# Kernel optimization log

Measured on AMD Instinct MI355X. Metric: run time of the kernel, lower is better.

Reference implementation:

```python
import jax, jax.numpy as jnp
import numpy as np

V, D, M, C, L = 100000, 256, 4096, 4096, 32
PAD = 0
EPS = 1e-8  # torch CosineSimilarity default eps


def setup_inputs() -> dict:
    key = jax.random.key(0)
    ks = jax.random.split(key, 6)
    xs = jax.random.randint(ks[0], (1, L), 0, V)
    mems = jax.random.randint(ks[1], (M, L), 0, V)
    ys = jax.random.randint(ks[2], (1, L), 0, V)
    cands = jax.random.randint(ks[3], (C, L), 0, V)
    lt = jax.random.normal(ks[4], (V, D), dtype=jnp.float32) * 0.02
    lt = lt.at[PAD].set(0.0)  # nn.Embedding padding_idx row is zero
    freqs = jax.random.uniform(ks[5], (V,), dtype=jnp.float32, minval=0.05, maxval=1.0)
    return {"xs": xs, "mems": mems, "ys": ys, "cands": cands, "lt": lt, "freqs": freqs}


def _encode(tokens, lt, freqs):
    # Batched Encoder.forward: freq-weighted average of token embeddings.
    # tokens: [N, L] -> [N, D]
    emb = lt[tokens]                       # [N, L, D] gather
    w = freqs[tokens]                      # [N, L]
    w = w / jnp.linalg.norm(w, axis=1, keepdims=True)  # w * (1 / ||w||)
    return jnp.einsum('nl,nld->nd', w, emb)


def reference(xs, mems, ys, cands, lt, freqs):
    xs_emb = _encode(xs, lt, freqs)                                   # [1, D]
    mems_enc = jnp.concatenate([_encode(mems, lt, freqs), xs_emb], 0)  # [M+1, D]
    # cosine similarity of xs_emb (broadcast) against each memory row
    an = jnp.maximum(jnp.linalg.norm(xs_emb, axis=1), EPS)            # [1]
    bn = jnp.maximum(jnp.linalg.norm(mems_enc, axis=1), EPS)          # [M+1]
    cos = (mems_enc @ xs_emb[0]) / (an * bn)                          # [M+1]
    att = jax.nn.softmax(cos)[None, :]                                # [1, M+1]
    lhs_emb = att @ mems_enc                                          # [1, D]
    ys_emb = _encode(ys, lt, freqs)                                   # [1, D]
    cand_emb = _encode(cands, lt, freqs)                              # [C, D]
    # torch.cat of lhs_emb repeated (1 + C) times; ys then cand encodings
    xs_out = jnp.tile(lhs_emb, (cands.shape[0] + 1, 1))               # [C+1, D]
    ys_out = jnp.concatenate([ys_emb, cand_emb], axis=0)              # [C+1, D]
    return xs_out, ys_out
```

## Files before the change

kernel.cpp:

```cpp
#include <hip/hip_runtime.h>

#define V_ 100000
#define D_ 256
#define M_ 4096
#define C_ 4096
#define L_ 32
#define ROWS_MEMS (M_ + 1)
#define NTASK (1 + M_ + 1 + C_)

__device__ __forceinline__ float wave_allreduce_sum(float v) {
    #pragma unroll
    for (int off = 32; off >= 1; off >>= 1) v += __shfl_xor(v, off, 64);
    return v;
}

__global__ __launch_bounds__(256) void encode_fused(
    const int* __restrict__ xs, const int* __restrict__ mems,
    const int* __restrict__ ys, const int* __restrict__ cands,
    const float* __restrict__ lt, const float* __restrict__ freqs,
    float* __restrict__ lhs_raw,
    float* __restrict__ gsum,
    float* __restrict__ out_ys)
{
    __shared__ float s_xf[D_];
    __shared__ float s_an2;
    __shared__ float s_lred[D_];
    __shared__ float s_ered;

    const int wave = threadIdx.x >> 6;
    const int lane = threadIdx.x & 63;
    const int d0 = lane * 4;
    const int rt0 = blockIdx.x * 4;
    const bool block_has_att = (rt0 <= M_);

    s_lred[threadIdx.x] = 0.f;
    if (threadIdx.x == 0) s_ered = 0.f;

    if (block_has_att && wave == 0) {
        int txs = 0; float wxs = 0.f;
        if (lane < L_) { txs = xs[lane]; wxs = freqs[txs]; }
        const float sx = wave_allreduce_sum(wxs * wxs);
        const float wnx = wxs / sqrtf(sx);
        float4 xf = make_float4(0.f, 0.f, 0.f, 0.f);
        #pragma unroll
        for (int l = 0; l < L_; ++l) {
            const int t = __shfl(txs, l, 64);
            const float wl = __shfl(wnx, l, 64);
            const float4 v = *reinterpret_cast<const float4*>(lt + (size_t)t * D_ + d0);
            xf.x += wl * v.x; xf.y += wl * v.y; xf.z += wl * v.z; xf.w += wl * v.w;
        }
        *reinterpret_cast<float4*>(&s_xf[d0]) = xf;
        const float an2 = wave_allreduce_sum(xf.x*xf.x + xf.y*xf.y + xf.z*xf.z + xf.w*xf.w);
        if (lane == 0) s_an2 = an2;
    }
    __syncthreads();

    const int rt = rt0 + wave;
    if (rt < NTASK) {
        const int* tok_ptr; float* dst = nullptr; bool has_att = false;
        if (rt == 0) {
            tok_ptr = xs; has_att = true;
        } else if (rt <= M_) {
            tok_ptr = mems + (size_t)(rt - 1) * L_; has_att = true;
        } else if (rt == M_ + 1) {
            tok_ptr = ys; dst = out_ys;
        } else {
            const int c = rt - (M_ + 2);
            tok_ptr = cands + (size_t)c * L_;
            dst = out_ys + (size_t)(c + 1) * D_;
        }

        int tok = 0; float w = 0.f;
        if (lane < L_) { tok = tok_ptr[lane]; w = freqs[tok]; }
        const float s2 = wave_allreduce_sum(w * w);
        const float wn = w / sqrtf(s2);

        float4 acc = make_float4(0.f, 0.f, 0.f, 0.f);
        #pragma unroll
        for (int l = 0; l < L_; ++l) {
            const int t = __shfl(tok, l, 64);
            const float wl = __shfl(wn, l, 64);
            const float4 v = *reinterpret_cast<const float4*>(lt + (size_t)t * D_ + d0);
            acc.x += wl * v.x; acc.y += wl * v.y; acc.z += wl * v.z; acc.w += wl * v.w;
        }

        if (has_att) {
            const float4 xf = *reinterpret_cast<const float4*>(&s_xf[d0]);
            const float d = wave_allreduce_sum(acc.x*xf.x + acc.y*xf.y + acc.z*xf.z + acc.w*xf.w);
            const float q = wave_allreduce_sum(acc.x*acc.x + acc.y*acc.y + acc.z*acc.z + acc.w*acc.w);
            const float an = fmaxf(sqrtf(s_an2), 1e-8f);
            const float bn = fmaxf(sqrtf(q),  1e-8f);
            const float e = expf(d / (an * bn));
            atomicAdd(&s_lred[d0 + 0], e * acc.x);
            atomicAdd(&s_lred[d0 + 1], e * acc.y);
            atomicAdd(&s_lred[d0 + 2], e * acc.z);
            atomicAdd(&s_lred[d0 + 3], e * acc.w);
            if (lane == 0) atomicAdd(&s_ered, e);
        } else {
            *reinterpret_cast<float4*>(dst + d0) = acc;
        }
    }

    if (block_has_att) {
        __syncthreads();
        atomicAdd(&lhs_raw[threadIdx.x], s_lred[threadIdx.x]);
        if (threadIdx.x == 0) atomicAdd(gsum, s_ered);
    }
}

__global__ __launch_bounds__(256) void finalize_tile(
    const float* __restrict__ lhs_raw, const float* __restrict__ gsum,
    float* __restrict__ out_xs)
{
    const float val = lhs_raw[threadIdx.x] / gsum[0];
    for (int r = blockIdx.x; r < ROWS_MEMS; r += gridDim.x)
        out_xs[(size_t)r * D_ + threadIdx.x] = val;
}

extern "C" void kernel_launch(void* const* d_in, const int* in_sizes, int n_in,
                              void* d_out, int out_size, void* d_ws, size_t ws_size,
                              hipStream_t stream) {
    const int*   xs    = (const int*)d_in[0];
    const int*   mems  = (const int*)d_in[1];
    const int*   ys    = (const int*)d_in[2];
    const int*   cands = (const int*)d_in[3];
    const float* lt    = (const float*)d_in[4];
    const float* freqs = (const float*)d_in[5];

    float* out    = (float*)d_out;
    float* out_xs = out;
    float* out_ys = out + (size_t)ROWS_MEMS * D_;

    float* lhs_raw = (float*)d_ws;
    float* gsum    = lhs_raw + D_;

    hipMemsetAsync(lhs_raw, 0, (D_ + 1) * sizeof(float), stream);

    encode_fused<<<(NTASK + 3) / 4, 256, 0, stream>>>(xs, mems, ys, cands, lt, freqs,
                                                      lhs_raw, gsum, out_ys);
    finalize_tile<<<1024, 256, 0, stream>>>(lhs_raw, gsum, out_xs);
}
```

Baseline: 188.5 us.

## Process two encode tasks per wave and compute norms with scalar loads

The fused encode kernel now launches half as many blocks, and each wave handles two rows: one from the first half of the task range and one candidate row from the second half. Their gather loops are interleaved to expose more independent memory loads per wave. Token weights are now read with uniform per-row scalar loads in place of lane loads plus shuffles. Every block recomputes the xs encoding and always does the shared-memory and global atomic reduction, which adds redundant work and atomics in blocks that have no attention rows. Fewer waves in flight may reduce latency hiding.

```diff
diff --git a/kernel.cpp b/kernel.cpp
--- a/kernel.cpp
+++ b/kernel.cpp
@@ -7,6 +7,8 @@
 #define L_ 32
 #define ROWS_MEMS (M_ + 1)
 #define NTASK (1 + M_ + 1 + C_)
+#define NBLK 1025
+#define HALF (NBLK * 4)
 
 __device__ __forceinline__ float wave_allreduce_sum(float v) {
     #pragma unroll
@@ -14,7 +16,7 @@
     return v;
 }
 
-__global__ __launch_bounds__(256) void encode_fused(
+__global__ __launch_bounds__(256, 4) void encode_fused(
     const int* __restrict__ xs, const int* __restrict__ mems,
     const int* __restrict__ ys, const int* __restrict__ cands,
     const float* __restrict__ lt, const float* __restrict__ freqs,
@@ -30,22 +32,21 @@
     const int wave = threadIdx.x >> 6;
     const int lane = threadIdx.x & 63;
     const int d0 = lane * 4;
-    const int rt0 = blockIdx.x * 4;
-    const bool block_has_att = (rt0 <= M_);
+    const int g = blockIdx.x * 4 + wave;
 
     s_lred[threadIdx.x] = 0.f;
     if (threadIdx.x == 0) s_ered = 0.f;
 
-    if (block_has_att && wave == 0) {
-        int txs = 0; float wxs = 0.f;
-        if (lane < L_) { txs = xs[lane]; wxs = freqs[txs]; }
-        const float sx = wave_allreduce_sum(wxs * wxs);
-        const float wnx = wxs / sqrtf(sx);
+    if (wave == 0) {
+        float s2 = 0.f;
+        #pragma unroll
+        for (int l = 0; l < L_; ++l) { const float w = freqs[xs[l]]; s2 += w * w; }
+        const float inv = 1.0f / sqrtf(s2);
         float4 xf = make_float4(0.f, 0.f, 0.f, 0.f);
         #pragma unroll
         for (int l = 0; l < L_; ++l) {
-            const int t = __shfl(txs, l, 64);
-            const float wl = __shfl(wnx, l, 64);
+            const int t = xs[l];
+            const float wl = freqs[t] * inv;
             const float4 v = *reinterpret_cast<const float4*>(lt + (size_t)t * D_ + d0);
             xf.x += wl * v.x; xf.y += wl * v.y; xf.z += wl * v.z; xf.w += wl * v.w;
         }
@@ -55,57 +56,69 @@
     }
     __syncthreads();
 
-    const int rt = rt0 + wave;
-    if (rt < NTASK) {
-        const int* tok_ptr; float* dst = nullptr; bool has_att = false;
-        if (rt == 0) {
-            tok_ptr = xs; has_att = true;
-        } else if (rt <= M_) {
-            tok_ptr = mems + (size_t)(rt - 1) * L_; has_att = true;
-        } else if (rt == M_ + 1) {
-            tok_ptr = ys; dst = out_ys;
-        } else {
-            const int c = rt - (M_ + 2);
-            tok_ptr = cands + (size_t)c * L_;
-            dst = out_ys + (size_t)(c + 1) * D_;
-        }
-
-        int tok = 0; float w = 0.f;
-        if (lane < L_) { tok = tok_ptr[lane]; w = freqs[tok]; }
-        const float s2 = wave_allreduce_sum(w * w);
-        const float wn = w / sqrtf(s2);
-
-        float4 acc = make_float4(0.f, 0.f, 0.f, 0.f);
-        #pragma unroll
-        for (int l = 0; l < L_; ++l) {
-            const int t = __shfl(tok, l, 64);
-            const float wl = __shfl(wn, l, 64);
-            const float4 v = *reinterpret_cast<const float4*>(lt + (size_t)t * D_ + d0);
-            acc.x += wl * v.x; acc.y += wl * v.y; acc.z += wl * v.z; acc.w += wl * v.w;
-        }
-
-        if (has_att) {
-            const float4 xf = *reinterpret_cast<const float4*>(&s_xf[d0]);
-            const float d = wave_allreduce_sum(acc.x*xf.x + acc.y*xf.y + acc.z*xf.z + acc.w*xf.w);
-            const float q = wave_allreduce_sum(acc.x*acc.x + acc.y*acc.y + acc.z*acc.z + acc.w*acc.w);
-            const float an = fmaxf(sqrtf(s_an2), 1e-8f);
-            const float bn = fmaxf(sqrtf(q),  1e-8f);
-            const float e = expf(d / (an * bn));
-            atomicAdd(&s_lred[d0 + 0], e * acc.x);
-            atomicAdd(&s_lred[d0 + 1], e * acc.y);
-            atomicAdd(&s_lred[d0 + 2], e * acc.z);
-            atomicAdd(&s_lred[d0 + 3], e * acc.w);
-            if (lane == 0) atomicAdd(&s_ered, e);
-        } else {
-            *reinterpret_cast<float4*>(dst + d0) = acc;
-        }
+    const int rtA = g;
+    const int* tpA; float* dstA = nullptr; int aiA = -1;
+    if (rtA == 0) {
+        tpA = xs; aiA = M_;
+    } else if (rtA <= M_) {
+        tpA = mems + (size_t)(rtA - 1) * L_; aiA = rtA - 1;
+    } else if (rtA == M_ + 1) {
+        tpA = ys; dstA = out_ys;
+    } else {
+        const int c = rtA - (M_ + 2);
+        tpA = cands + (size_t)c * L_;
+        dstA = out_ys + (size_t)(c + 1) * D_;
     }
 
-    if (block_has_att) {
-        __syncthreads();
-        atomicAdd(&lhs_raw[threadIdx.x], s_lred[threadIdx.x]);
-        if (threadIdx.x == 0) atomicAdd(gsum, s_ered);
+    const int rtB = g + HALF;
+    const bool hasB = (rtB < NTASK);
+    const int cB = hasB ? (rtB - (M_ + 2)) : 0;
+    const int* tpB = cands + (size_t)cB * L_;
+    float* dstB = out_ys + (size_t)(cB + 1) * D_;
+
+    float s2A = 0.f, s2B = 0.f;
+    #pragma unroll
+    for (int l = 0; l < L_; ++l) {
+        const float wa = freqs[tpA[l]]; s2A += wa * wa;
+        const float wb = freqs[tpB[l]]; s2B += wb * wb;
     }
+    const float invA = 1.0f / sqrtf(s2A);
+    const float invB = 1.0f / sqrtf(s2B);
+
+    float4 accA = make_float4(0.f, 0.f, 0.f, 0.f);
+    float4 accB = make_float4(0.f, 0.f, 0.f, 0.f);
+    #pragma unroll
+    for (int l = 0; l < L_; ++l) {
+        const int ta = tpA[l];
+        const int tb = tpB[l];
+        const float wa = freqs[ta] * invA;
+        const float wb = freqs[tb] * invB;
+        const float4 va = *reinterpret_cast<const float4*>(lt + (size_t)ta * D_ + d0);
+        const float4 vb = *reinterpret_cast<const float4*>(lt + (size_t)tb * D_ + d0);
+        accA.x += wa * va.x; accA.y += wa * va.y; accA.z += wa * va.z; accA.w += wa * va.w;
+        accB.x += wb * vb.x; accB.y += wb * vb.y; accB.z += wb * vb.z; accB.w += wb * vb.w;
+    }
+
+    if (aiA >= 0) {
+        const float4 xf = *reinterpret_cast<const float4*>(&s_xf[d0]);
+        const float d = wave_allreduce_sum(accA.x*xf.x + accA.y*xf.y + accA.z*xf.z + accA.w*xf.w);
+        const float q = wave_allreduce_sum(accA.x*accA.x + accA.y*accA.y + accA.z*accA.z + accA.w*accA.w);
+        const float an = fmaxf(sqrtf(s_an2), 1e-8f);
+        const float bn = fmaxf(sqrtf(q),  1e-8f);
+        const float e = expf(d / (an * bn));
+        atomicAdd(&s_lred[d0 + 0], e * accA.x);
+        atomicAdd(&s_lred[d0 + 1], e * accA.y);
+        atomicAdd(&s_lred[d0 + 2], e * accA.z);
+        atomicAdd(&s_lred[d0 + 3], e * accA.w);
+        if (lane == 0) atomicAdd(&s_ered, e);
+    } else {
+        *reinterpret_cast<float4*>(dstA + d0) = accA;
+    }
+    if (hasB) *reinterpret_cast<float4*>(dstB + d0) = accB;
+
+    __syncthreads();
+    atomicAdd(&lhs_raw[threadIdx.x], s_lred[threadIdx.x]);
+    if (threadIdx.x == 0) atomicAdd(gsum, s_ered);
 }
 
 __global__ __launch_bounds__(256) void finalize_tile(
@@ -136,7 +149,7 @@
 
     hipMemsetAsync(lhs_raw, 0, (D_ + 1) * sizeof(float), stream);
 
-    encode_fused<<<(NTASK + 3) / 4, 256, 0, stream>>>(xs, mems, ys, cands, lt, freqs,
-                                                      lhs_raw, gsum, out_ys);
+    encode_fused<<<NBLK, 256, 0, stream>>>(xs, mems, ys, cands, lt, freqs,
+                                           lhs_raw, gsum, out_ys);
     finalize_tile<<<1024, 256, 0, stream>>>(lhs_raw, gsum, out_xs);
 }
```

Measured after the change: 221.6 us. +17.6%, slower.
